# Optimization experiments

Hardware: AMD Instinct MI355X
Metric: run time of the kernel (lower is better)

## Reference

```python
import jax, jax.numpy as jnp
import numpy as np

ENC_DIM, DEC_DIM, ATT_DIM = 2048, 512, 512
B, P = 256, 196


def setup_inputs() -> dict:
    key = jax.random.key(0)
    ks = jax.random.split(key, 8)
    s_e = 1.0 / np.sqrt(ENC_DIM)
    s_d = 1.0 / np.sqrt(DEC_DIM)
    s_a = 1.0 / np.sqrt(ATT_DIM)
    return {
        "encoder_out": jax.random.normal(ks[0], (B, P, ENC_DIM), jnp.float32),
        "decoder_hidden": jax.random.normal(ks[1], (1, B, DEC_DIM), jnp.float32),
        "We_w": jax.random.uniform(ks[2], (ENC_DIM, ATT_DIM), jnp.float32, -s_e, s_e),
        "We_b": jax.random.uniform(ks[3], (ATT_DIM,), jnp.float32, -s_e, s_e),
        "Wd_w": jax.random.uniform(ks[4], (DEC_DIM, ATT_DIM), jnp.float32, -s_d, s_d),
        "Wd_b": jax.random.uniform(ks[5], (ATT_DIM,), jnp.float32, -s_d, s_d),
        "Wf_w": jax.random.uniform(ks[6], (ATT_DIM,), jnp.float32, -s_a, s_a),
        "Wf_b": jax.random.uniform(ks[7], (), jnp.float32, -s_a, s_a),
    }


def reference(encoder_out, decoder_hidden, We_w, We_b, Wd_w, Wd_b, Wf_w, Wf_b):
    # decoder_hidden: (1, B, D) -> (B, 1, D)
    dh = jnp.transpose(decoder_hidden, (1, 0, 2))
    att1 = jnp.einsum("bpe,ea->bpa", encoder_out, We_w) + We_b      # (B, P, A)
    att2 = jnp.einsum("bqd,da->bqa", dh, Wd_w) + Wd_b               # (B, 1, A)
    h = jax.nn.relu(att1 + att2)                                     # (B, P, A)
    att = jnp.einsum("bpa,a->bp", h, Wf_w) + Wf_b                    # (B, P)
    alpha = jax.nn.softmax(att, axis=1)                              # (B, P)
    awe = jnp.einsum("bpe,bp->be", encoder_out, alpha)               # (B, E)
    return (awe, alpha)
```

## Files before the change

### kernel.cpp

```cpp
#include <hip/hip_runtime.h>

#define BB   256
#define PP   196
#define ED   2048
#define AD   512
#define MROWS (BB * PP)
#define AWE_ELEMS (BB * ED)
#define ALPHA_ELEMS (BB * PP)

typedef __bf16 bf16x8 __attribute__((ext_vector_type(8)));
typedef float  f32x4  __attribute__((ext_vector_type(4)));

__device__ __forceinline__ f32x4 mfma16(bf16x8 a, bf16x8 b, f32x4 c) {
    return __builtin_amdgcn_mfma_f32_16x16x32_bf16(a, b, c, 0, 0, 0);
}

__device__ __forceinline__ bf16x8 pack8(float4 a, float4 b) {
    bf16x8 r;
    r[0] = (__bf16)a.x; r[1] = (__bf16)a.y; r[2] = (__bf16)a.z; r[3] = (__bf16)a.w;
    r[4] = (__bf16)b.x; r[5] = (__bf16)b.y; r[6] = (__bf16)b.z; r[7] = (__bf16)b.w;
    return r;
}


__global__ void zero_att_k(float4* __restrict__ att4) {
    att4[blockIdx.x * 256 + threadIdx.x] = make_float4(0.f, 0.f, 0.f, 0.f);
}

__global__ void wet_k(const float* __restrict__ We, unsigned short* __restrict__ WeT) {
    int idx = blockIdx.x * 256 + threadIdx.x;
    int n = idx >> 11;
    int k = idx & 2047;
    __bf16 h = (__bf16)We[k * AD + n];
    WeT[idx] = __builtin_bit_cast(unsigned short, h);
}

__global__ void att2_k(const float* __restrict__ dh, const float* __restrict__ Wd,
                       const float* __restrict__ Wd_b, const float* __restrict__ We_b,
                       float* __restrict__ att2p) {
    int b = blockIdx.x;
    int t = threadIdx.x;
    __shared__ float dhs[512];
    dhs[t]       = dh[b * 512 + t];
    dhs[t + 256] = dh[b * 512 + 256 + t];
    __syncthreads();
    float a0 = 0.f, a1 = 0.f;
    #pragma unroll 4
    for (int d = 0; d < 512; d++) {
        float x = dhs[d];
        a0 = fmaf(x, Wd[d * AD + t], a0);
        a1 = fmaf(x, Wd[d * AD + 256 + t], a1);
    }
    att2p[b * AD + t]       = a0 + Wd_b[t]       + We_b[t];
    att2p[b * AD + 256 + t] = a1 + Wd_b[t + 256] + We_b[t + 256];
}

__global__ __launch_bounds__(256) void gemm_att(
    const float* __restrict__ enc, const unsigned short* __restrict__ WeT,
    const float* __restrict__ att2p, const float* __restrict__ Wf,
    float* __restrict__ att)
{
    __shared__ alignas(16) unsigned short As[128 * 64];
    __shared__ alignas(16) unsigned short Bs[128 * 64];

    const int tid  = threadIdx.x;
    const int wave = tid >> 6;
    const int lane = tid & 63;
    const int lr   = lane & 15;
    const int quad = lane >> 4;
    const int rq = (wave & 1) * 64;
    const int cq = (wave >> 1) * 64;
    const int row_base = blockIdx.x * 128;
    const int n_base   = blockIdx.y * 128;

    f32x4 acc[4][4];
    #pragma unroll
    for (int i = 0; i < 4; i++)
        #pragma unroll
        for (int j = 0; j < 4; j++)
            acc[i][j] = (f32x4){0.f, 0.f, 0.f, 0.f};

    const int arow  = tid >> 1;
    const int akoff = (tid & 1) * 32;
    const float* aptr = enc + (size_t)(row_base + arow) * ED + akoff;
    bf16x8* awr = (bf16x8*)&As[arow * 64 + akoff];

    const unsigned short* bsrc = WeT + (size_t)n_base * ED;

    for (int kb = 0; kb < ED; kb += 64) {
        #pragma unroll
        for (int i = 0; i < 4; i++) {
            int c = wave * 4 + i;
            int n = c * 8 + (lane >> 3);
            const unsigned short* src = bsrc + (size_t)n * ED + kb + (lane & 7) * 8;
            unsigned short* dst = &Bs[c * 512];
            __builtin_amdgcn_global_load_lds(
                (const __attribute__((address_space(1))) void*)src,
                (__attribute__((address_space(3))) void*)dst, 16, 0, 0);
        }
        const float4* ap = (const float4*)(aptr + kb);
        float4 f0 = ap[0], f1 = ap[1], f2 = ap[2], f3 = ap[3];
        float4 f4 = ap[4], f5 = ap[5], f6 = ap[6], f7 = ap[7];
        awr[0] = pack8(f0, f1);
        awr[1] = pack8(f2, f3);
        awr[2] = pack8(f4, f5);
        awr[3] = pack8(f6, f7);

        __syncthreads();

        #pragma unroll
        for (int ks = 0; ks < 2; ks++) {
            bf16x8 af[4], bfr[4];
            #pragma unroll
            for (int i = 0; i < 4; i++)
                af[i] = *(const bf16x8*)&As[(rq + i * 16 + lr) * 64 + ks * 32 + quad * 8];
            #pragma unroll
            for (int j = 0; j < 4; j++)
                bfr[j] = *(const bf16x8*)&Bs[(cq + j * 16 + lr) * 64 + ks * 32 + quad * 8];
            #pragma unroll
            for (int i = 0; i < 4; i++)
                #pragma unroll
                for (int j = 0; j < 4; j++)
                    acc[i][j] = mfma16(af[i], bfr[j], acc[i][j]);
        }
        __syncthreads();
    }

    float wf[4];
    int colg[4];
    #pragma unroll
    for (int j = 0; j < 4; j++) {
        colg[j] = n_base + cq + j * 16 + lr;
        wf[j] = Wf[colg[j]];
    }
    #pragma unroll
    for (int i = 0; i < 4; i++) {
        int row0 = row_base + rq + i * 16 + quad * 4;
        #pragma unroll
        for (int r = 0; r < 4; r++) {
            int row = row0 + r;
            unsigned bidx = (unsigned)row / 196u;
            const float* bias = att2p + bidx * AD;
            float s = 0.f;
            #pragma unroll
            for (int j = 0; j < 4; j++) {
                float v = acc[i][j][r] + bias[colg[j]];
                v = fmaxf(v, 0.f);
                s = fmaf(v, wf[j], s);
            }
            s += __shfl_xor(s, 1);
            s += __shfl_xor(s, 2);
            s += __shfl_xor(s, 4);
            s += __shfl_xor(s, 8);
            if (lr == 0) atomicAdd(&att[row], s);
        }
    }
}

__global__ void softmax_k(const float* __restrict__ att, float* __restrict__ alpha) {
    int b = blockIdx.x;
    int l = threadIdx.x;
    float v[4];
    float m = -1e30f;
    #pragma unroll
    for (int i = 0; i < 4; i++) {
        int p = l + i * 64;
        v[i] = (p < PP) ? att[b * PP + p] : -1e30f;
        m = fmaxf(m, v[i]);
    }
    #pragma unroll
    for (int off = 32; off > 0; off >>= 1) m = fmaxf(m, __shfl_xor(m, off));
    float s = 0.f;
    #pragma unroll
    for (int i = 0; i < 4; i++) {
        int p = l + i * 64;
        v[i] = (p < PP) ? __expf(v[i] - m) : 0.f;
        s += v[i];
    }
    #pragma unroll
    for (int off = 32; off > 0; off >>= 1) s += __shfl_xor(s, off);
    float inv = 1.0f / s;
    #pragma unroll
    for (int i = 0; i < 4; i++) {
        int p = l + i * 64;
        if (p < PP) alpha[b * PP + p] = v[i] * inv;
    }
}

__global__ __launch_bounds__(256) void awe_k(const float* __restrict__ enc,
                                             const float* __restrict__ alpha,
                                             float* __restrict__ awe) {
    int b = blockIdx.x;
    int ec = blockIdx.y;
    int t = threadIdx.x;
    __shared__ float al[PP];
    if (t < PP) al[t] = alpha[b * PP + t];
    __syncthreads();

    const float4* bp = (const float4*)enc + ((size_t)b * PP * (ED / 4) + ec * 256 + t);
    float4 acc = make_float4(0.f, 0.f, 0.f, 0.f);
    #pragma unroll 4
    for (int p = 0; p < PP; p++) {
        float a = al[p];
        float4 x = bp[(size_t)p * (ED / 4)];
        acc.x = fmaf(a, x.x, acc.x);
        acc.y = fmaf(a, x.y, acc.y);
        acc.z = fmaf(a, x.z, acc.z);
        acc.w = fmaf(a, x.w, acc.w);
    }
    float4* ow = (float4*)awe + ((size_t)b * (ED / 4) + ec * 256 + t);
    *ow = acc;
}

extern "C" void kernel_launch(void* const* d_in, const int* in_sizes, int n_in,
                              void* d_out, int out_size, void* d_ws, size_t ws_size,
                              hipStream_t stream) {
    const float* enc  = (const float*)d_in[0];
    const float* dh   = (const float*)d_in[1];
    const float* We   = (const float*)d_in[2];
    const float* We_b = (const float*)d_in[3];
    const float* Wd   = (const float*)d_in[4];
    const float* Wd_b = (const float*)d_in[5];
    const float* Wf   = (const float*)d_in[6];

    float* out = (float*)d_out;

    float*          att   = (float*)d_ws;
    unsigned short* WeT   = (unsigned short*)((char*)d_ws + 262144);
    float*          att2p = (float*)((char*)d_ws + 262144 + 2097152);

    zero_att_k<<<49, 256, 0, stream>>>((float4*)att);
    wet_k<<<4096, 256, 0, stream>>>(We, WeT);
    att2_k<<<256, 256, 0, stream>>>(dh, Wd, Wd_b, We_b, att2p);
    gemm_att<<<dim3(392, 4), 256, 0, stream>>>(enc, WeT, att2p, Wf, att);
    softmax_k<<<256, 64, 0, stream>>>(att, out + AWE_ELEMS);
    awe_k<<<dim3(256, 2), 256, 0, stream>>>(enc, out + AWE_ELEMS, out);
}
```

Measured before the change: 988.3 us.

## Swizzle LDS tiles, remap GEMM blocks across XCDs, tile the weight transpose

The GEMM's shared-memory A and B tiles now use an XOR swizzle on their 16-byte chunks, applied both on write (including the direct global-to-LDS loads for B) and on the MFMA fragment reads, to cut LDS bank conflicts. The grid is flattened and each block id is remapped so that the four N-tiles of a row group run on the same XCD, improving L2 reuse of the encoder rows. The weight transpose kernel now goes through a padded shared-memory tile, giving coalesced reads and writes instead of strided single-element accesses. The swizzle adds index arithmetic and must stay consistent between the load and read sides.

```diff
diff --git a/kernel.cpp b/kernel.cpp
--- a/kernel.cpp
+++ b/kernel.cpp
@@ -4,9 +4,7 @@
 #define PP   196
 #define ED   2048
 #define AD   512
-#define MROWS (BB * PP)
 #define AWE_ELEMS (BB * ED)
-#define ALPHA_ELEMS (BB * PP)
 
 typedef __bf16 bf16x8 __attribute__((ext_vector_type(8)));
 typedef float  f32x4  __attribute__((ext_vector_type(4)));
@@ -22,17 +20,40 @@
     return r;
 }
 
+__device__ __forceinline__ unsigned short bfbits(float x) {
+    return __builtin_bit_cast(unsigned short, (__bf16)x);
+}
+
 
 __global__ void zero_att_k(float4* __restrict__ att4) {
     att4[blockIdx.x * 256 + threadIdx.x] = make_float4(0.f, 0.f, 0.f, 0.f);
 }
 
 __global__ void wet_k(const float* __restrict__ We, unsigned short* __restrict__ WeT) {
-    int idx = blockIdx.x * 256 + threadIdx.x;
-    int n = idx >> 11;
-    int k = idx & 2047;
-    __bf16 h = (__bf16)We[k * AD + n];
-    WeT[idx] = __builtin_bit_cast(unsigned short, h);
+    __shared__ unsigned short S[64][72];
+    const int t  = threadIdx.x;
+    const int k0 = blockIdx.x * 64;
+    const int n0 = blockIdx.y * 64;
+
+    const int rr = t >> 4;
+    const int c4 = t & 15;
+    #pragma unroll
+    for (int i = 0; i < 4; i++) {
+        int kr = i * 16 + rr;
+        float4 v = *(const float4*)&We[(size_t)(k0 + kr) * AD + n0 + c4 * 4];
+        S[c4 * 4 + 0][kr] = bfbits(v.x);
+        S[c4 * 4 + 1][kr] = bfbits(v.y);
+        S[c4 * 4 + 2][kr] = bfbits(v.z);
+        S[c4 * 4 + 3][kr] = bfbits(v.w);
+    }
+    __syncthreads();
+
+    const int n = t >> 2;
+    #pragma unroll
+    for (int c = 0; c < 2; c++) {
+        int ch = (t & 3) * 2 + c;
+        *(uint4*)&WeT[(size_t)(n0 + n) * ED + k0 + ch * 8] = *(const uint4*)&S[n][ch * 8];
+    }
 }
 
 __global__ void att2_k(const float* __restrict__ dh, const float* __restrict__ Wd,
@@ -68,10 +89,17 @@
     const int lane = tid & 63;
     const int lr   = lane & 15;
     const int quad = lane >> 4;
+    const int swz  = lr & 7;
     const int rq = (wave & 1) * 64;
     const int cq = (wave >> 1) * 64;
-    const int row_base = blockIdx.x * 128;
-    const int n_base   = blockIdx.y * 128;
+
+    const int id  = blockIdx.x;
+    const int xcd = id & 7;
+    const int t2  = id >> 3;
+    const int ny  = t2 & 3;
+    const int rg  = t2 >> 2;
+    const int row_base = (rg * 8 + xcd) * 128;
+    const int n_base   = ny * 128;
 
     f32x4 acc[4][4];
     #pragma unroll
@@ -83,16 +111,17 @@
     const int arow  = tid >> 1;
     const int akoff = (tid & 1) * 32;
     const float* aptr = enc + (size_t)(row_base + arow) * ED + akoff;
-    bf16x8* awr = (bf16x8*)&As[arow * 64 + akoff];
+    const int asw = arow & 7;
 
     const unsigned short* bsrc = WeT + (size_t)n_base * ED;
+    const int bn  = lane >> 3;
+    const int bjj = (lane & 7) ^ bn;
 
     for (int kb = 0; kb < ED; kb += 64) {
         #pragma unroll
         for (int i = 0; i < 4; i++) {
             int c = wave * 4 + i;
-            int n = c * 8 + (lane >> 3);
-            const unsigned short* src = bsrc + (size_t)n * ED + kb + (lane & 7) * 8;
+            const unsigned short* src = bsrc + (size_t)(c * 8 + bn) * ED + kb + bjj * 8;
             unsigned short* dst = &Bs[c * 512];
             __builtin_amdgcn_global_load_lds(
                 (const __attribute__((address_space(1))) void*)src,
@@ -101,22 +130,26 @@
         const float4* ap = (const float4*)(aptr + kb);
         float4 f0 = ap[0], f1 = ap[1], f2 = ap[2], f3 = ap[3];
         float4 f4 = ap[4], f5 = ap[5], f6 = ap[6], f7 = ap[7];
-        awr[0] = pack8(f0, f1);
-        awr[1] = pack8(f2, f3);
-        awr[2] = pack8(f4, f5);
-        awr[3] = pack8(f6, f7);
+        {
+            int lc0 = (tid & 1) * 4;
+            *(bf16x8*)&As[arow * 64 + ((lc0 + 0) ^ asw) * 8] = pack8(f0, f1);
+            *(bf16x8*)&As[arow * 64 + ((lc0 + 1) ^ asw) * 8] = pack8(f2, f3);
+            *(bf16x8*)&As[arow * 64 + ((lc0 + 2) ^ asw) * 8] = pack8(f4, f5);
+            *(bf16x8*)&As[arow * 64 + ((lc0 + 3) ^ asw) * 8] = pack8(f6, f7);
+        }
 
         __syncthreads();
 
         #pragma unroll
         for (int ks = 0; ks < 2; ks++) {
             bf16x8 af[4], bfr[4];
+            int pc = ((ks * 4 + quad) ^ swz) * 8;
             #pragma unroll
             for (int i = 0; i < 4; i++)
-                af[i] = *(const bf16x8*)&As[(rq + i * 16 + lr) * 64 + ks * 32 + quad * 8];
+                af[i] = *(const bf16x8*)&As[(rq + i * 16 + lr) * 64 + pc];
             #pragma unroll
             for (int j = 0; j < 4; j++)
-                bfr[j] = *(const bf16x8*)&Bs[(cq + j * 16 + lr) * 64 + ks * 32 + quad * 8];
+                bfr[j] = *(const bf16x8*)&Bs[(cq + j * 16 + lr) * 64 + pc];
             #pragma unroll
             for (int i = 0; i < 4; i++)
                 #pragma unroll
@@ -230,9 +263,9 @@
     float*          att2p = (float*)((char*)d_ws + 262144 + 2097152);
 
     zero_att_k<<<49, 256, 0, stream>>>((float4*)att);
-    wet_k<<<4096, 256, 0, stream>>>(We, WeT);
+    wet_k<<<dim3(32, 8), 256, 0, stream>>>(We, WeT);
     att2_k<<<256, 256, 0, stream>>>(dh, Wd, Wd_b, We_b, att2p);
-    gemm_att<<<dim3(392, 4), 256, 0, stream>>>(enc, WeT, att2p, Wf, att);
+    gemm_att<<<1568, 256, 0, stream>>>(enc, WeT, att2p, Wf, att);
     softmax_k<<<256, 64, 0, stream>>>(att, out + AWE_ELEMS);
     awe_k<<<dim3(256, 2), 256, 0, stream>>>(enc, out + AWE_ELEMS, out);
 }
```

Measured after the change: 859.0 us. -13.1%, faster.
